# Kernel optimization log

Measured on AMD Instinct MI355X. Metric: run time of the kernel, lower is better.

The kernel has to match this reference:

```python
import jax, jax.numpy as jnp
import numpy as np

T, B, H, V = 128, 32, 1024, 32000


def setup_inputs() -> dict:
    key = jax.random.key(0)
    ks = jax.random.split(key, 8)
    scale = 1.0 / np.sqrt(H)
    return {
        "input": jax.random.normal(ks[0], (T, B, H), dtype=jnp.float32),
        "hidden": jnp.zeros((B, H), dtype=jnp.float32),
        "w_ic": jax.random.uniform(ks[1], (H, H), jnp.float32, -scale, scale),
        "w_ix": jax.random.uniform(ks[2], (H, H), jnp.float32, -scale, scale),
        "w_fc": jax.random.uniform(ks[3], (H, H), jnp.float32, -scale, scale),
        "w_fx": jax.random.uniform(ks[4], (H, H), jnp.float32, -scale, scale),
        "b_i": jnp.zeros((H,), dtype=jnp.float32),
        "b_f": jnp.zeros((H,), dtype=jnp.float32),
        "W_out": jax.random.uniform(ks[5], (V, H), jnp.float32, -scale, scale),
        "b_out": jnp.zeros((V,), dtype=jnp.float32),
    }


def reference(input, hidden, w_ic, w_ix, w_fc, w_fx, b_i, b_f, W_out, b_out):
    # Precompute input projections for all timesteps: [T, B, H]
    ix = jnp.einsum("tbh,kh->tbk", input, w_ix)
    fx = jnp.einsum("tbh,kh->tbk", input, w_fx)

    def step(c, xs):
        ix_t, fx_t, x_t = xs
        i_t = jax.nn.sigmoid(c @ w_ic.T + b_i + ix_t)
        f_t = jax.nn.sigmoid(c @ w_fc.T + b_f + fx_t)
        c_new = i_t * x_t + f_t * c  # RAN gated-additive update
        return c_new, c_new

    hidden_final, outputs = jax.lax.scan(step, hidden, (ix, fx, input))
    logits = jnp.einsum("tbh,vh->tbv", outputs, W_out) + b_out
    log_probs = jax.nn.log_softmax(logits, axis=-1)
    return log_probs, hidden_final
```

## Files before the change

### kernel.cpp

```cpp
#include <hip/hip_runtime.h>

typedef __attribute__((ext_vector_type(4))) float f32x4;
typedef __attribute__((ext_vector_type(8))) short bf16x8;

#define T_DIM 128
#define B_DIM 32
#define H_DIM 1024
#define V_DIM 32000
#define MROWS 4096
#define NBLK 64
#define CLSLOT (B_DIM*H_DIM)
#define WSTRIDE 1028

__device__ __forceinline__ ushort f2bf(float f){
  union { float f; unsigned u; } x; x.f = f;
  unsigned u = x.u;
  unsigned r = (u + 0x7fffu + ((u >> 16) & 1u)) >> 16;
  return (ushort)r;
}
__device__ __forceinline__ float bf2f(ushort h){
  union { unsigned u; float f; } x; x.u = ((unsigned)h) << 16;
  return x.f;
}

__device__ __forceinline__ void async_copy16(void* lds, const void* g){
  __builtin_amdgcn_global_load_lds((const __attribute__((address_space(1))) void*)g,
                                   (__attribute__((address_space(3))) void*)lds, 16, 0, 0);
}

__global__ void cast_bf16_kernel(const float* __restrict__ s, ushort* __restrict__ d, int n4){
  int stride = gridDim.x * blockDim.x;
  for (int i = blockIdx.x*blockDim.x + threadIdx.x; i < n4; i += stride){
    float4 v = ((const float4*)s)[i];
    ushort4 o = make_ushort4(f2bf(v.x), f2bf(v.y), f2bf(v.z), f2bf(v.w));
    ((ushort4*)d)[i] = o;
  }
}

__global__ void cast_split_kernel(const float* __restrict__ s, ushort* __restrict__ dh,
                                  ushort* __restrict__ dl, int n4){
  int stride = gridDim.x * blockDim.x;
  for (int i = blockIdx.x*blockDim.x + threadIdx.x; i < n4; i += stride){
    float4 v = ((const float4*)s)[i];
    ushort4 h = make_ushort4(f2bf(v.x), f2bf(v.y), f2bf(v.z), f2bf(v.w));
    ushort4 l = make_ushort4(f2bf(v.x - bf2f(h.x)), f2bf(v.y - bf2f(h.y)),
                             f2bf(v.z - bf2f(h.z)), f2bf(v.w - bf2f(h.w)));
    ((ushort4*)dh)[i] = h;
    ((ushort4*)dl)[i] = l;
  }
}

__global__ __launch_bounds__(256) void gemm_bt(
    const ushort* __restrict__ A, const ushort* __restrict__ B,
    float* __restrict__ C, const float* __restrict__ bias,
    int N, int K, int NTN, int order,
    float* __restrict__ pmax, float* __restrict__ psum)
{
  __shared__ ushort lA[128*32];
  __shared__ ushort lB[128*32];
  __shared__ float pmS[4][64], psS[4][64];
  int tid = threadIdx.x;
  int lane = tid & 63, wid = tid >> 6;
  int bid = blockIdx.x;
  int tm, tn;
  if (order){
    int xcd = bid & 7, id = bid >> 3;
    tn = id >> 2;
    tm = (xcd << 2) | (id & 3);
  } else {
    tm = bid / NTN; tn = bid % NTN;
  }
  int row0 = tm << 7, col0 = tn << 7;

  f32x4 acc[4][4] = {};

  auto stage = [&](const ushort* __restrict__ g, ushort* l, int r0, int k0){
    int c = wid << 1;
    const ushort* s0 = g + (size_t)(r0 + (c<<4) + (lane>>2))*K + k0 + ((lane&3)<<3);
    async_copy16(l + (c<<9), s0);
    async_copy16(l + ((c+1)<<9), s0 + (size_t)16*K);
  };

  int nk = K >> 5;
  stage(A, lA, row0, 0);
  stage(B, lB, col0, 0);
  int wm = (wid >> 1) << 6, wn = (wid & 1) << 6;
  int kg = (lane >> 4) << 3;
  int ar = lane & 15;

  for (int kt = 0; kt < nk; ++kt){
    __syncthreads();
    bf16x8 af[4], bfr[4];
    #pragma unroll
    for (int mi = 0; mi < 4; ++mi) af[mi]  = *(const bf16x8*)&lA[(wm + mi*16 + ar)*32 + kg];
    #pragma unroll
    for (int ni = 0; ni < 4; ++ni) bfr[ni] = *(const bf16x8*)&lB[(wn + ni*16 + ar)*32 + kg];
    #pragma unroll
    for (int mi = 0; mi < 4; ++mi)
      #pragma unroll
      for (int ni = 0; ni < 4; ++ni)
        acc[mi][ni] = __builtin_amdgcn_mfma_f32_16x16x32_bf16(af[mi], bfr[ni], acc[mi][ni], 0, 0, 0);
    if (kt + 1 < nk){
      __syncthreads();
      stage(A, lA, row0, (kt+1) << 5);
      stage(B, lB, col0, (kt+1) << 5);
    }
  }

  int rr = (lane >> 4) << 2;
  float bb4[4];
  #pragma unroll
  for (int ni = 0; ni < 4; ++ni) bb4[ni] = bias ? bias[col0 + wn + ni*16 + ar] : 0.f;

  #pragma unroll
  for (int mi = 0; mi < 4; ++mi){
    #pragma unroll
    for (int q = 0; q < 4; ++q){
      int r = row0 + wm + mi*16 + rr + q;
      float vals[4];
      #pragma unroll
      for (int ni = 0; ni < 4; ++ni){
        vals[ni] = acc[mi][ni][q] + bb4[ni];
        C[(size_t)r * N + col0 + wn + ni*16 + ar] = vals[ni];
      }
      if (pmax){
        float m = fmaxf(fmaxf(vals[0], vals[1]), fmaxf(vals[2], vals[3]));
        #pragma unroll
        for (int o = 1; o < 16; o <<= 1) m = fmaxf(m, __shfl_xor(m, o));
        float s = expf(vals[0]-m) + expf(vals[1]-m) + expf(vals[2]-m) + expf(vals[3]-m);
        #pragma unroll
        for (int o = 1; o < 16; o <<= 1) s += __shfl_xor(s, o);
        if (ar == 0){ int rl = mi*16 + rr + q; pmS[wid][rl] = m; psS[wid][rl] = s; }
      }
    }
  }
  if (pmax){
    __syncthreads();
    if (tid < 128){
      int rl = tid & 63, half = tid >> 6;
      int w0 = half*2, w1 = w0 + 1;
      float m0 = pmS[w0][rl], m1 = pmS[w1][rl];
      float s0 = psS[w0][rl], s1 = psS[w1][rl];
      float M = fmaxf(m0, m1);
      float S = s0*expf(m0-M) + s1*expf(m1-M);
      int r = row0 + half*64 + rl;
      pmax[(size_t)r*NTN + tn] = M;
      psum[(size_t)r*NTN + tn] = S;
    }
  }
}

__global__ __launch_bounds__(256) void gemm_bt_split(
    const ushort* __restrict__ Ah, const ushort* __restrict__ Al,
    const ushort* __restrict__ Bh, const ushort* __restrict__ Bl,
    float* __restrict__ C, int N, int K, int NTN)
{
  __shared__ ushort lAh[128*32], lAl[128*32], lBh[128*32], lBl[128*32];
  int tid = threadIdx.x;
  int lane = tid & 63, wid = tid >> 6;
  int tm = blockIdx.x / NTN, tn = blockIdx.x % NTN;
  int row0 = tm << 7, col0 = tn << 7;

  f32x4 acc[4][4] = {};

  auto stage = [&](const ushort* __restrict__ g, ushort* l, int r0, int k0){
    int c = wid << 1;
    const ushort* s0 = g + (size_t)(r0 + (c<<4) + (lane>>2))*K + k0 + ((lane&3)<<3);
    async_copy16(l + (c<<9), s0);
    async_copy16(l + ((c+1)<<9), s0 + (size_t)16*K);
  };

  int nk = K >> 5;
  stage(Ah, lAh, row0, 0); stage(Al, lAl, row0, 0);
  stage(Bh, lBh, col0, 0); stage(Bl, lBl, col0, 0);
  int wm = (wid >> 1) << 6, wn = (wid & 1) << 6;
  int kg = (lane >> 4) << 3;
  int ar = lane & 15;

  for (int kt = 0; kt < nk; ++kt){
    __syncthreads();
    bf16x8 afh[4], afl[4], bfh[4], bfl[4];
    #pragma unroll
    for (int mi = 0; mi < 4; ++mi){
      afh[mi] = *(const bf16x8*)&lAh[(wm + mi*16 + ar)*32 + kg];
      afl[mi] = *(const bf16x8*)&lAl[(wm + mi*16 + ar)*32 + kg];
    }
    #pragma unroll
    for (int ni = 0; ni < 4; ++ni){
      bfh[ni] = *(const bf16x8*)&lBh[(wn + ni*16 + ar)*32 + kg];
      bfl[ni] = *(const bf16x8*)&lBl[(wn + ni*16 + ar)*32 + kg];
    }
    #pragma unroll
    for (int mi = 0; mi < 4; ++mi)
      #pragma unroll
      for (int ni = 0; ni < 4; ++ni){
        acc[mi][ni] = __builtin_amdgcn_mfma_f32_16x16x32_bf16(afh[mi], bfh[ni], acc[mi][ni], 0, 0, 0);
        acc[mi][ni] = __builtin_amdgcn_mfma_f32_16x16x32_bf16(afh[mi], bfl[ni], acc[mi][ni], 0, 0, 0);
        acc[mi][ni] = __builtin_amdgcn_mfma_f32_16x16x32_bf16(afl[mi], bfh[ni], acc[mi][ni], 0, 0, 0);
      }
    if (kt + 1 < nk){
      __syncthreads();
      stage(Ah, lAh, row0, (kt+1) << 5); stage(Al, lAl, row0, (kt+1) << 5);
      stage(Bh, lBh, col0, (kt+1) << 5); stage(Bl, lBl, col0, (kt+1) << 5);
    }
  }

  int rr = (lane >> 4) << 2;
  #pragma unroll
  for (int mi = 0; mi < 4; ++mi)
    #pragma unroll
    for (int ni = 0; ni < 4; ++ni){
      int r  = row0 + wm + mi*16 + rr;
      int cc = col0 + wn + ni*16 + ar;
      #pragma unroll
      for (int q = 0; q < 4; ++q)
        C[(size_t)(r + q) * N + cc] = acc[mi][ni][q];
    }
}

__global__ __launch_bounds__(512) void ran_all(
    const ushort* __restrict__ ch_init, const ushort* __restrict__ cl_init,
    ushort* __restrict__ cl_all, const float* __restrict__ hidden,
    const ushort* __restrict__ wh, const ushort* __restrict__ wl,
    const float* __restrict__ b_i, const float* __restrict__ b_f,
    const float* __restrict__ ixfx, const float* __restrict__ x_all,
    ushort* __restrict__ out_bf, float* __restrict__ hid_final,
    unsigned* __restrict__ bar)
{
  __shared__ ushort lWh[32*WSTRIDE];
  __shared__ ushort lWl[32*WSTRIDE];
  __shared__ float part[8][64][4];
  __shared__ float gsm[2*32*17];
  __shared__ float cfl[32][17];

  int tid = threadIdx.x, lane = tid & 63, wid = tid >> 6;
  int kh = wid & 1, mh = (wid >> 1) & 1, gate = wid >> 2;
  int nb = blockIdx.x << 4;
  int ar = lane & 15, kg = (lane >> 4) << 3;
  int um8 = tid >> 3, ukp = (tid & 7) << 1;

  #pragma unroll
  for (int u = 0; u < 8; ++u){
    int unit = u*512 + tid;
    int r = unit >> 7, off = (unit & 127) << 3;
    int g = r >> 4, c = r & 15;
    size_t gsrc = (size_t)((g<<10) + nb + c) * H_DIM + off;
    *(bf16x8*)&lWh[r*WSTRIDE + off] = *(const bf16x8*)&wh[gsrc];
    *(bf16x8*)&lWl[r*WSTRIDE + off] = *(const bf16x8*)&wl[gsrc];
  }
  if (tid < 256){
    cfl[um8][ukp]   = hidden[(um8<<10) + nb + ukp];
    cfl[um8][ukp+1] = hidden[(um8<<10) + nb + ukp + 1];
  }
  float bb = (gate ? b_f : b_i)[nb + ar];
  const ushort* bbase_h = &lWh[((gate<<4) + ar)*WSTRIDE + (kh<<9)];
  const ushort* bbase_l = &lWl[((gate<<4) + ar)*WSTRIDE + (kh<<9)];
  __syncthreads();

  for (int t = 0; t < T_DIM; ++t){
    const ushort* ah = t ? out_bf + (size_t)(t-1)*CLSLOT : ch_init;
    const ushort* al = t ? cl_all + (size_t)(t-1)*CLSLOT : cl_init;
    ushort* clw   = cl_all + (size_t)t*CLSLOT;
    ushort* out_t = out_bf + (size_t)t*CLSLOT;
    const float* ixfx_t = ixfx + (size_t)t * (B_DIM*2048);
    const float* x_t    = x_all + (size_t)t * (B_DIM*H_DIM);

    float2 xv2;
    if (tid < 256) xv2 = *(const float2*)&x_t[(um8<<10) + nb + ukp];
    float pix[4];
    if (kh == 0){
      #pragma unroll
      for (int q = 0; q < 4; ++q){
        int m = (mh<<4) + ((lane>>4)<<2) + q;
        pix[q] = ixfx_t[m*2048 + (gate<<10) + nb + ar];
      }
    }

    const ushort* arow_h = ah + (size_t)((mh<<4) + ar) * H_DIM + (kh<<9);
    const ushort* arow_l = al + (size_t)((mh<<4) + ar) * H_DIM + (kh<<9);
    f32x4 a0 = {}, a1 = {}, a2 = {};
    #pragma unroll 4
    for (int kk = 0; kk < 16; ++kk){
      int o = (kk<<5) + kg;
      bf16x8 vah = *(const bf16x8*)&arow_h[o];
      bf16x8 val = *(const bf16x8*)&arow_l[o];
      bf16x8 vbh = *(const bf16x8*)&bbase_h[o];
      bf16x8 vbl = *(const bf16x8*)&bbase_l[o];
      a0 = __builtin_amdgcn_mfma_f32_16x16x32_bf16(vah, vbh, a0, 0, 0, 0);
      a1 = __builtin_amdgcn_mfma_f32_16x16x32_bf16(vah, vbl, a1, 0, 0, 0);
      a2 = __builtin_amdgcn_mfma_f32_16x16x32_bf16(val, vbh, a2, 0, 0, 0);
    }
    f32x4 acc = a0 + a1 + a2;
    *(f32x4*)&part[wid][lane][0] = acc;
    __syncthreads();
    if (kh == 0){
      f32x4 sum = *(const f32x4*)&part[wid][lane][0] + *(const f32x4*)&part[wid+1][lane][0];
      #pragma unroll
      for (int q = 0; q < 4; ++q){
        int m = (mh<<4) + ((lane>>4)<<2) + q;
        float pre = sum[q] + bb + pix[q];
        gsm[((gate<<5) + m)*17 + ar] = 1.f / (1.f + expf(-pre));
      }
    }
    __syncthreads();
    if (tid < 256){
      int colb = (um8<<10) + nb + ukp;
      float iv0 = gsm[um8*17 + ukp],        iv1 = gsm[um8*17 + ukp + 1];
      float fv0 = gsm[(32+um8)*17 + ukp],   fv1 = gsm[(32+um8)*17 + ukp + 1];
      float c0 = cfl[um8][ukp], c1 = cfl[um8][ukp+1];
      float n0 = iv0*xv2.x + fv0*c0;
      float n1 = iv1*xv2.y + fv1*c1;
      cfl[um8][ukp] = n0; cfl[um8][ukp+1] = n1;
      ushort h0 = f2bf(n0), h1 = f2bf(n1);
      unsigned hp = (unsigned)h0 | ((unsigned)h1 << 16);
      unsigned lp = (unsigned)f2bf(n0 - bf2f(h0)) | ((unsigned)f2bf(n1 - bf2f(h1)) << 16);
      __hip_atomic_store((unsigned*)&out_t[colb], hp, __ATOMIC_RELAXED, __HIP_MEMORY_SCOPE_AGENT);
      __hip_atomic_store((unsigned*)&clw[colb],   lp, __ATOMIC_RELAXED, __HIP_MEMORY_SCOPE_AGENT);
      if (t == T_DIM-1){ hid_final[colb] = n0; hid_final[colb+1] = n1; }
    }
    if (t < T_DIM-1){
      __syncthreads();
      if (tid == 0){
        __hip_atomic_fetch_add(bar, 1u, __ATOMIC_RELAXED, __HIP_MEMORY_SCOPE_AGENT);
        unsigned target = (unsigned)NBLK * (unsigned)(t + 1);
        while (__hip_atomic_load(bar, __ATOMIC_RELAXED, __HIP_MEMORY_SCOPE_AGENT) < target)
          __builtin_amdgcn_s_sleep(1);
      }
      __syncthreads();
    }
  }
}

__global__ void init_c_kernel(const float* __restrict__ hidden,
                              ushort* __restrict__ ch, ushort* __restrict__ cl,
                              unsigned* __restrict__ bar){
  int i = blockIdx.x * blockDim.x + threadIdx.x;
  if (i == 0) *bar = 0;
  float v = hidden[i];
  ushort h = f2bf(v);
  ch[i] = h;
  cl[i] = f2bf(v - bf2f(h));
}

__global__ __launch_bounds__(64) void lse_reduce(const float* __restrict__ pmax,
                                                 const float* __restrict__ psum,
                                                 float* __restrict__ lse, int ntn){
  int row = blockIdx.x, lane = threadIdx.x;
  float m = -1e30f, s = 0.f;
  for (int i = lane; i < ntn; i += 64){
    float mi = pmax[(size_t)row*ntn + i], si = psum[(size_t)row*ntn + i];
    float M = fmaxf(m, mi);
    s = s*expf(m - M) + si*expf(mi - M);
    m = M;
  }
  #pragma unroll
  for (int o = 32; o; o >>= 1){
    float m2 = __shfl_xor(m, o), s2 = __shfl_xor(s, o);
    float M = fmaxf(m, m2);
    s = s*expf(m - M) + s2*expf(m2 - M);
    m = M;
  }
  if (lane == 0) lse[row] = m + logf(s);
}

__global__ __launch_bounds__(256) void sub_kernel(float* __restrict__ logits,
                                                  const float* __restrict__ lse){
  size_t row = blockIdx.x;
  float l = lse[row];
  float4* p4 = (float4*)(logits + row * (size_t)V_DIM);
  for (int i = threadIdx.x; i < V_DIM/4; i += 256){
    float4 v = p4[i];
    v.x -= l; v.y -= l; v.z -= l; v.w -= l;
    p4[i] = v;
  }
}

extern "C" void kernel_launch(void* const* d_in, const int* in_sizes, int n_in,
                              void* d_out, int out_size, void* d_ws, size_t ws_size,
                              hipStream_t stream)
{
  const float* input  = (const float*)d_in[0];
  const float* hidden = (const float*)d_in[1];
  const float* w_ic   = (const float*)d_in[2];
  const float* w_ix   = (const float*)d_in[3];
  const float* w_fc   = (const float*)d_in[4];
  const float* w_fx   = (const float*)d_in[5];
  const float* b_i    = (const float*)d_in[6];
  const float* b_f    = (const float*)d_in[7];
  const float* W_out  = (const float*)d_in[8];
  const float* b_out  = (const float*)d_in[9];
  float* out = (float*)d_out;

  char* ws = (char*)d_ws;
  ushort* wout_bf = (ushort*)(ws + 0);
  ushort* in_hi   = (ushort*)(ws + 65536000);
  ushort* in_lo   = (ushort*)(ws + 73924608);
  ushort* wx_hi   = (ushort*)(ws + 82313216);
  ushort* wx_lo   = (ushort*)(ws + 86507520);
  ushort* wc_hi   = (ushort*)(ws + 90701824);
  ushort* wc_lo   = (ushort*)(ws + 94896128);
  ushort* out_bf  = (ushort*)(ws + 99090432);
  unsigned* bar   = (unsigned*)(ws + 107479040);
  ushort* ch_init = (ushort*)(ws + 107479296);
  ushort* cl_init = (ushort*)(ws + 107544832);
  ushort* cl_all  = in_hi;
  float*  pmax    = (float*)in_lo;
  float*  psum    = (float*)(ws + 78020608);
  float*  lse     = (float*)wx_hi;
  float*  ixfx    = out;

  cast_bf16_kernel <<<2048,256,0,stream>>>(W_out, wout_bf, V_DIM*H_DIM/4);
  cast_split_kernel<<<1024,256,0,stream>>>(input, in_hi, in_lo, MROWS*H_DIM/4);
  cast_split_kernel<<<256,256,0,stream>>>(w_ix, wx_hi,             wx_lo,             H_DIM*H_DIM/4);
  cast_split_kernel<<<256,256,0,stream>>>(w_fx, wx_hi+H_DIM*H_DIM, wx_lo+H_DIM*H_DIM, H_DIM*H_DIM/4);
  cast_split_kernel<<<256,256,0,stream>>>(w_ic, wc_hi,             wc_lo,             H_DIM*H_DIM/4);
  cast_split_kernel<<<256,256,0,stream>>>(w_fc, wc_hi+H_DIM*H_DIM, wc_lo+H_DIM*H_DIM, H_DIM*H_DIM/4);

  gemm_bt_split<<<32*16,256,0,stream>>>(in_hi, in_lo, wx_hi, wx_lo, ixfx, 2048, H_DIM, 16);

  init_c_kernel<<<128,256,0,stream>>>(hidden, ch_init, cl_init, bar);

  ran_all<<<NBLK,512,0,stream>>>(ch_init, cl_init, cl_all, hidden, wc_hi, wc_lo, b_i, b_f,
                                 ixfx, input, out_bf, out + (size_t)MROWS*V_DIM, bar);

  gemm_bt<<<32*250,256,0,stream>>>(out_bf, wout_bf, out, b_out, V_DIM, H_DIM, 250, 1, pmax, psum);
  lse_reduce<<<MROWS,64,0,stream>>>(pmax, psum, lse, 250);
  sub_kernel<<<MROWS,256,0,stream>>>(out, lse);
}
```

Before: 2.031 ms.

## Replace atomic counter barrier with per-block flags and blocked recurrent state layout

```diff
diff --git a/kernel.cpp b/kernel.cpp
--- a/kernel.cpp
+++ b/kernel.cpp
@@ -10,6 +10,7 @@
 #define MROWS 4096
 #define NBLK 64
 #define CLSLOT (B_DIM*H_DIM)
+#define CSTEP 65536
 #define WSTRIDE 1028
 
 __device__ __forceinline__ ushort f2bf(float f){
@@ -219,13 +220,12 @@
 }
 
 __global__ __launch_bounds__(512) void ran_all(
-    const ushort* __restrict__ ch_init, const ushort* __restrict__ cl_init,
-    ushort* __restrict__ cl_all, const float* __restrict__ hidden,
+    const ushort* __restrict__ cinit, ushort* __restrict__ cstate,
     const ushort* __restrict__ wh, const ushort* __restrict__ wl,
     const float* __restrict__ b_i, const float* __restrict__ b_f,
     const float* __restrict__ ixfx, const float* __restrict__ x_all,
     ushort* __restrict__ out_bf, float* __restrict__ hid_final,
-    unsigned* __restrict__ bar)
+    unsigned* __restrict__ slots)
 {
   __shared__ ushort lWh[32*WSTRIDE];
   __shared__ ushort lWl[32*WSTRIDE];
@@ -235,7 +235,8 @@
 
   int tid = threadIdx.x, lane = tid & 63, wid = tid >> 6;
   int kh = wid & 1, mh = (wid >> 1) & 1, gate = wid >> 2;
-  int nb = blockIdx.x << 4;
+  int bid = blockIdx.x;
+  int nb = bid << 4;
   int ar = lane & 15, kg = (lane >> 4) << 3;
   int um8 = tid >> 3, ukp = (tid & 7) << 1;
 
@@ -248,44 +249,88 @@
     *(bf16x8*)&lWh[r*WSTRIDE + off] = *(const bf16x8*)&wh[gsrc];
     *(bf16x8*)&lWl[r*WSTRIDE + off] = *(const bf16x8*)&wl[gsrc];
   }
-  if (tid < 256){
-    cfl[um8][ukp]   = hidden[(um8<<10) + nb + ukp];
-    cfl[um8][ukp+1] = hidden[(um8<<10) + nb + ukp + 1];
-  }
   float bb = (gate ? b_f : b_i)[nb + ar];
   const ushort* bbase_h = &lWh[((gate<<4) + ar)*WSTRIDE + (kh<<9)];
   const ushort* bbase_l = &lWl[((gate<<4) + ar)*WSTRIDE + (kh<<9)];
+  int abase = (kh<<15) + ((kg>>4)<<10) + (((mh<<4) + ar)<<4) + (kg & 8);
   __syncthreads();
+  if (tid < 256){
+    float h0 = 0.f, h1 = 0.f;
+    h0 = ((const float*)nullptr == nullptr) ? 0.f : 0.f;
+    cfl[um8][ukp]   = x_all ? 0.f : 0.f;
+  }
+  if (tid < 256){
+    const float* hsrc = hid_final;
+  }
+  __syncthreads();
+
+  for (int t = 0; t < T_DIM; ++t){ (void)t; break; }
+
+}
+
+__global__ __launch_bounds__(512) void ran_all2(
+    const ushort* __restrict__ cinit, ushort* __restrict__ cstate,
+    const float* __restrict__ hiddenf,
+    const ushort* __restrict__ wh, const ushort* __restrict__ wl,
+    const float* __restrict__ b_i, const float* __restrict__ b_f,
+    const float* __restrict__ ixfx, const float* __restrict__ x_all,
+    ushort* __restrict__ out_bf, float* __restrict__ hid_final,
+    unsigned* __restrict__ slots)
+{
+  __shared__ ushort lWh[32*WSTRIDE];
+  __shared__ ushort lWl[32*WSTRIDE];
+  __shared__ float part[8][64][4];
+  __shared__ float gsm[2*32*17];
+  __shared__ float cfl[32][17];
+
+  int tid = threadIdx.x, lane = tid & 63, wid = tid >> 6;
+  int kh = wid & 1, mh = (wid >> 1) & 1, gate = wid >> 2;
+  int bid = blockIdx.x;
+  int nb = bid << 4;
+  int ar = lane & 15, kg = (lane >> 4) << 3;
+  int um8 = tid >> 3, ukp = (tid & 7) << 1;
+
+  #pragma unroll
+  for (int u = 0; u < 8; ++u){
+    int unit = u*512 + tid;
+    int r = unit >> 7, off = (unit & 127) << 3;
+    int g = r >> 4, c = r & 15;
+    size_t gsrc = (size_t)((g<<10) + nb + c) * H_DIM + off;
+    *(bf16x8*)&lWh[r*WSTRIDE + off] = *(const bf16x8*)&wh[gsrc];
+    *(bf16x8*)&lWl[r*WSTRIDE + off] = *(const bf16x8*)&wl[gsrc];
+  }
+  if (tid < 256){
+    cfl[um8][ukp]   = hiddenf[(um8<<10) + nb + ukp];
+    cfl[um8][ukp+1] = hiddenf[(um8<<10) + nb + ukp + 1];
+  }
+  float bb = (gate ? b_f : b_i)[nb + ar];
+  const ushort* bbase_h = &lWh[((gate<<4) + ar)*WSTRIDE + (kh<<9)];
+  const ushort* bbase_l = &lWl[((gate<<4) + ar)*WSTRIDE + (kh<<9)];
+  int abase = (kh<<15) + ((kg>>4)<<10) + (((mh<<4) + ar)<<4) + (kg & 8);
+  __syncthreads();
+
+  float2 xv2; float pix[4];
+  if (tid < 256) xv2 = *(const float2*)&x_all[(um8<<10) + nb + ukp];
+  if (kh == 0){
+    #pragma unroll
+    for (int q = 0; q < 4; ++q){
+      int m = (mh<<4) + ((lane>>4)<<2) + q;
+      pix[q] = ixfx[m*2048 + (gate<<10) + nb + ar];
+    }
+  }
 
   for (int t = 0; t < T_DIM; ++t){
-    const ushort* ah = t ? out_bf + (size_t)(t-1)*CLSLOT : ch_init;
-    const ushort* al = t ? cl_all + (size_t)(t-1)*CLSLOT : cl_init;
-    ushort* clw   = cl_all + (size_t)t*CLSLOT;
-    ushort* out_t = out_bf + (size_t)t*CLSLOT;
-    const float* ixfx_t = ixfx + (size_t)t * (B_DIM*2048);
-    const float* x_t    = x_all + (size_t)t * (B_DIM*H_DIM);
-
-    float2 xv2;
-    if (tid < 256) xv2 = *(const float2*)&x_t[(um8<<10) + nb + ukp];
-    float pix[4];
-    if (kh == 0){
-      #pragma unroll
-      for (int q = 0; q < 4; ++q){
-        int m = (mh<<4) + ((lane>>4)<<2) + q;
-        pix[q] = ixfx_t[m*2048 + (gate<<10) + nb + ar];
-      }
-    }
-
-    const ushort* arow_h = ah + (size_t)((mh<<4) + ar) * H_DIM + (kh<<9);
-    const ushort* arow_l = al + (size_t)((mh<<4) + ar) * H_DIM + (kh<<9);
+    const ushort* cst = t ? cstate + (size_t)(t-1)*CSTEP : cinit;
+
     f32x4 a0 = {}, a1 = {}, a2 = {};
     #pragma unroll 4
     for (int kk = 0; kk < 16; ++kk){
-      int o = (kk<<5) + kg;
-      bf16x8 vah = *(const bf16x8*)&arow_h[o];
-      bf16x8 val = *(const bf16x8*)&arow_l[o];
-      bf16x8 vbh = *(const bf16x8*)&bbase_h[o];
-      bf16x8 vbl = *(const bf16x8*)&bbase_l[o];
+      int oa = abase + (kk<<11);
+      int ob = (kk<<5) + kg;
+      bf16x8 vah = *(const bf16x8*)&cst[oa];
+      bf16x8 val = *(const bf16x8*)&cst[oa + 512];
+      bf16x8 vbh = *(const bf16x8*)&bbase_h[ob];
+      bf16x8 vbl = *(const bf16x8*)&bbase_l[ob];
       a0 = __builtin_amdgcn_mfma_f32_16x16x32_bf16(vah, vbh, a0, 0, 0, 0);
       a1 = __builtin_amdgcn_mfma_f32_16x16x32_bf16(vah, vbl, a1, 0, 0, 0);
       a2 = __builtin_amdgcn_mfma_f32_16x16x32_bf16(val, vbh, a2, 0, 0, 0);
@@ -304,9 +349,8 @@
     }
     __syncthreads();
     if (tid < 256){
-      int colb = (um8<<10) + nb + ukp;
-      float iv0 = gsm[um8*17 + ukp],        iv1 = gsm[um8*17 + ukp + 1];
-      float fv0 = gsm[(32+um8)*17 + ukp],   fv1 = gsm[(32+um8)*17 + ukp + 1];
+      float iv0 = gsm[um8*17 + ukp],       iv1 = gsm[um8*17 + ukp + 1];
+      float fv0 = gsm[(32+um8)*17 + ukp],  fv1 = gsm[(32+um8)*17 + ukp + 1];
       float c0 = cfl[um8][ukp], c1 = cfl[um8][ukp+1];
       float n0 = iv0*xv2.x + fv0*c0;
       float n1 = iv1*xv2.y + fv1*c1;
@@ -314,17 +358,36 @@
       ushort h0 = f2bf(n0), h1 = f2bf(n1);
       unsigned hp = (unsigned)h0 | ((unsigned)h1 << 16);
       unsigned lp = (unsigned)f2bf(n0 - bf2f(h0)) | ((unsigned)f2bf(n1 - bf2f(h1)) << 16);
-      __hip_atomic_store((unsigned*)&out_t[colb], hp, __ATOMIC_RELAXED, __HIP_MEMORY_SCOPE_AGENT);
-      __hip_atomic_store((unsigned*)&clw[colb],   lp, __ATOMIC_RELAXED, __HIP_MEMORY_SCOPE_AGENT);
-      if (t == T_DIM-1){ hid_final[colb] = n0; hid_final[colb+1] = n1; }
+      size_t cb = (size_t)t*CSTEP + (bid<<10) + (um8<<4) + ukp;
+      __hip_atomic_store((unsigned*)&cstate[cb],       hp, __ATOMIC_RELAXED, __HIP_MEMORY_SCOPE_AGENT);
+      __hip_atomic_store((unsigned*)&cstate[cb + 512], lp, __ATOMIC_RELAXED, __HIP_MEMORY_SCOPE_AGENT);
+      int rb = (um8<<10) + nb + ukp;
+      *(unsigned*)&out_bf[(size_t)t*CLSLOT + rb] = hp;
+      if (t == T_DIM-1){ hid_final[rb] = n0; hid_final[rb+1] = n1; }
     }
     if (t < T_DIM-1){
       __syncthreads();
-      if (tid == 0){
-        __hip_atomic_fetch_add(bar, 1u, __ATOMIC_RELAXED, __HIP_MEMORY_SCOPE_AGENT);
-        unsigned target = (unsigned)NBLK * (unsigned)(t + 1);
-        while (__hip_atomic_load(bar, __ATOMIC_RELAXED, __HIP_MEMORY_SCOPE_AGENT) < target)
+      if (tid == 0)
+        __hip_atomic_store(&slots[bid], (unsigned)(t+1), __ATOMIC_RELAXED, __HIP_MEMORY_SCOPE_AGENT);
+      {
+        const float* x_t  = x_all + (size_t)(t+1)*CLSLOT;
+        const float* ix_t = ixfx  + (size_t)(t+1)*(B_DIM*2048);
+        if (tid < 256) xv2 = *(const float2*)&x_t[(um8<<10) + nb + ukp];
+        if (kh == 0){
+          #pragma unroll
+          for (int q = 0; q < 4; ++q){
+            int m = (mh<<4) + ((lane>>4)<<2) + q;
+            pix[q] = ix_t[m*2048 + (gate<<10) + nb + ar];
+          }
+        }
+      }
+      if (wid == 0){
+        unsigned tgt = (unsigned)(t+1);
+        while (1){
+          unsigned v = __hip_atomic_load(&slots[lane], __ATOMIC_RELAXED, __HIP_MEMORY_SCOPE_AGENT);
+          if (__ballot(v < tgt) == 0ull) break;
           __builtin_amdgcn_s_sleep(1);
+        }
       }
       __syncthreads();
     }
@@ -332,14 +395,16 @@
 }
 
 __global__ void init_c_kernel(const float* __restrict__ hidden,
-                              ushort* __restrict__ ch, ushort* __restrict__ cl,
-                              unsigned* __restrict__ bar){
+                              ushort* __restrict__ cinit, unsigned* __restrict__ slots){
   int i = blockIdx.x * blockDim.x + threadIdx.x;
-  if (i == 0) *bar = 0;
+  if (blockIdx.x == 0 && threadIdx.x < NBLK) slots[threadIdx.x] = 0;
   float v = hidden[i];
   ushort h = f2bf(v);
-  ch[i] = h;
-  cl[i] = f2bf(v - bf2f(h));
+  ushort l = f2bf(v - bf2f(h));
+  int m = i >> 10, col = i & 1023;
+  int j = col >> 4, k = col & 15;
+  cinit[(j<<10) + (m<<4) + k]       = h;
+  cinit[(j<<10) + (m<<4) + k + 512] = l;
 }
 
 __global__ __launch_bounds__(64) void lse_reduce(const float* __restrict__ pmax,
@@ -400,12 +465,11 @@
   ushort* wc_hi   = (ushort*)(ws + 90701824);
   ushort* wc_lo   = (ushort*)(ws + 94896128);
   ushort* out_bf  = (ushort*)(ws + 99090432);
-  unsigned* bar   = (unsigned*)(ws + 107479040);
-  ushort* ch_init = (ushort*)(ws + 107479296);
-  ushort* cl_init = (ushort*)(ws + 107544832);
-  ushort* cl_all  = in_hi;
-  float*  pmax    = (float*)in_lo;
-  float*  psum    = (float*)(ws + 78020608);
+  unsigned* slots = (unsigned*)(ws + 107479040);
+  ushort* cinit   = (ushort*)(ws + 107479296);
+  ushort* cstate  = in_hi;
+  float*  pmax    = (float*)(ws + 65536000);
+  float*  psum    = (float*)(ws + 69632000);
   float*  lse     = (float*)wx_hi;
   float*  ixfx    = out;
 
@@ -418,10 +482,10 @@
 
   gemm_bt_split<<<32*16,256,0,stream>>>(in_hi, in_lo, wx_hi, wx_lo, ixfx, 2048, H_DIM, 16);
 
-  init_c_kernel<<<128,256,0,stream>>>(hidden, ch_init, cl_init, bar);
-
-  ran_all<<<NBLK,512,0,stream>>>(ch_init, cl_init, cl_all, hidden, wc_hi, wc_lo, b_i, b_f,
-                                 ixfx, input, out_bf, out + (size_t)MROWS*V_DIM, bar);
+  init_c_kernel<<<128,256,0,stream>>>(hidden, cinit, slots);
+
+  ran_all2<<<NBLK,512,0,stream>>>(cinit, cstate, hidden, wc_hi, wc_lo, b_i, b_f,
+                                  ixfx, input, out_bf, out + (size_t)MROWS*V_DIM, slots);
 
   gemm_bt<<<32*250,256,0,stream>>>(out_bf, wout_bf, out, b_out, V_DIM, H_DIM, 250, 1, pmax, psum);
   lse_reduce<<<MROWS,64,0,stream>>>(pmax, psum, lse, 250);
```

Result: no change. 2.052 ms (+1.0%).
